# Kernel tuning notes

Measured on AMD Instinct MI355X. Metric: run time of the kernel, lower is better.

Reference implementation:

```python
import jax, jax.numpy as jnp
import numpy as np

NUM_LEVELS = 4
RADIUS = 4


def _avg_pool2(x):
    # x: [N, H, W] -> [N, H//2, W//2], 2x2 mean pool, stride 2 (F.avg_pool2d(corr,2,2))
    N, H, W = x.shape
    return x.reshape(N, H // 2, 2, W // 2, 2).mean(axis=(2, 4))


def _bilinear_sample(img, x, y):
    # img: [N, H, W]; x, y: [N, P] pixel coords.
    # Matches F.grid_sample(..., mode='bilinear', align_corners=True, padding_mode='zeros')
    # after the pixel->normalized->pixel round trip in bilinear_sampler (identity).
    N, H, W = img.shape
    x0 = jnp.floor(x)
    y0 = jnp.floor(y)
    wx = x - x0
    wy = y - y0
    x0i = x0.astype(jnp.int32)
    y0i = y0.astype(jnp.int32)
    flat = img.reshape(N, H * W)

    def gather(yi, xi):
        valid = (xi >= 0) & (xi <= W - 1) & (yi >= 0) & (yi <= H - 1)
        idx = jnp.clip(yi, 0, H - 1) * W + jnp.clip(xi, 0, W - 1)
        v = jnp.take_along_axis(flat, idx, axis=1)
        return jnp.where(valid, v, jnp.zeros((), img.dtype))

    v00 = gather(y0i, x0i)
    v01 = gather(y0i, x0i + 1)
    v10 = gather(y0i + 1, x0i)
    v11 = gather(y0i + 1, x0i + 1)
    return (v00 * (1 - wy) * (1 - wx) + v01 * (1 - wy) * wx
            + v10 * wy * (1 - wx) + v11 * wy * wx)


def _corr_block(fmap1, fmap2, coords):
    B, D, H, W = fmap1.shape
    # all-pairs correlation: [B, H*W, H*W] / sqrt(D)
    f1 = fmap1.reshape(B, D, H * W)
    f2 = fmap2.reshape(B, D, H * W)
    corr = jnp.einsum('bdn,bdm->bnm', f1, f2) / jnp.sqrt(jnp.asarray(D, fmap1.dtype))
    corr = corr.reshape(B * H * W, H, W)
    pyramid = [corr]
    for _ in range(NUM_LEVELS - 1):
        corr = _avg_pool2(corr)
        pyramid.append(corr)

    # coords: [B, 2, H, W] (x, y) -> [B*H*W, 2]
    c = coords.transpose(0, 2, 3, 1).reshape(B * H * W, 2)
    r = RADIUS
    d = jnp.linspace(-r, r, 2 * r + 1)
    dyg, dxg = jnp.meshgrid(d, d, indexing='ij')
    # faithful to torch: delta = stack(meshgrid(dy, dx), -1); channel 0 added to x, 1 to y
    delta = jnp.stack([dyg, dxg], axis=-1).reshape(-1, 2)  # [81, 2]

    outs = []
    for i, lvl in enumerate(pyramid):
        cl = c[:, None, :] / (2.0 ** i) + delta[None, :, :]  # [N, 81, 2]
        s = _bilinear_sample(lvl, cl[..., 0], cl[..., 1])    # [N, 81]
        outs.append(s.reshape(B, H, W, (2 * r + 1) ** 2))
    out = jnp.concatenate(outs, axis=-1)                     # [B, H, W, 4*81]
    return out.transpose(0, 3, 1, 2).astype(jnp.float32)


def setup_inputs() -> dict:
    key = jax.random.key(0)
    k1, k2, k3 = jax.random.split(key, 3)
    B, D, H, W = 2, 256, 80, 80
    fmap1 = jax.random.normal(k1, (B, D, H, W), dtype=jnp.float32)
    fmap2 = jax.random.normal(k2, (B, D, H, W), dtype=jnp.float32)
    # pixel coords in [0, W-1] x [0, H-1] (channel 0 = x, channel 1 = y)
    u = jax.random.uniform(k3, (B, 2, H, W), dtype=jnp.float32)
    scale = jnp.asarray([W - 1, H - 1], jnp.float32).reshape(1, 2, 1, 1)
    coords = u * scale
    return {"fmap1": fmap1, "fmap2": fmap2, "coords": coords}


def reference(fmap1, fmap2, coords):
    return _corr_block(fmap1, fmap2, coords)
```

## Files before the change

kernel.cpp:

```cpp
#include <hip/hip_runtime.h>


typedef _Float16 h2 __attribute__((ext_vector_type(2)));
typedef _Float16 half8 __attribute__((ext_vector_type(8)));
typedef float f32x4 __attribute__((ext_vector_type(4)));

#define HWDIM 80
#define DCH 256
#define NPIX 12800
#define NBUCKET 800
#define CHP 352

__global__ __launch_bounds__(256) void zero_k(float4* __restrict__ dst) {
    int i = blockIdx.x * 256 + threadIdx.x;
    dst[i] = make_float4(0.f, 0.f, 0.f, 0.f);
}

__global__ __launch_bounds__(256) void transpose_all(const float* __restrict__ f1,
                                                     const float* __restrict__ f2,
                                                     _Float16* __restrict__ f1h,
                                                     _Float16* __restrict__ f2p0) {
    __shared__ float tile[256][33];
    int bid = blockIdx.x;
    bool isf1 = bid < 400;
    int lb = isf1 ? bid : bid - 400;
    const float* src = isf1 ? f1 : f2;
    int b = lb / 200;
    int s0 = (lb % 200) * 32;
    int t = threadIdx.x;
    const float* sb = src + (size_t)b * DCH * (HWDIM * HWDIM);
#pragma unroll 4
    for (int k = 0; k < 32; ++k) {
        int j = t + 256 * k;
        int c = j >> 5, s = j & 31;
        tile[c][s] = sb[(size_t)c * (HWDIM * HWDIM) + s0 + s];
    }
    __syncthreads();
    int p = t & 127;
    int srow = t >> 7;
    if (isf1) {
        _Float16* db = f1h + ((size_t)b * 6400 + s0) * DCH;
#pragma unroll 4
        for (int k = 0; k < 16; ++k) {
            int s = 2 * k + srow;
            h2 v;
            v[0] = (_Float16)tile[2 * p][s];
            v[1] = (_Float16)tile[2 * p + 1][s];
            *(h2*)(db + (size_t)s * DCH + 2 * p) = v;
        }
    } else {
#pragma unroll 4
        for (int k = 0; k < 16; ++k) {
            int s = 2 * k + srow;
            int spatial = s0 + s;
            int yy = spatial / 80;
            int xx = spatial - yy * 80;
            h2 v;
            v[0] = (_Float16)tile[2 * p][s];
            v[1] = (_Float16)tile[2 * p + 1][s];
            size_t off = (size_t)b * 2073600 + (size_t)(p >> 4) * 259200
                       + ((size_t)(yy + 5) * 90 + (xx + 5)) * 32 + ((2 * p) & 31);
            *(h2*)(f2p0 + off) = v;
        }
    }
}

__global__ __launch_bounds__(256) void pools(const _Float16* __restrict__ l0,
                                             _Float16* __restrict__ l1,
                                             _Float16* __restrict__ l2,
                                             _Float16* __restrict__ l3) {
    int i = blockIdx.x * 256 + threadIdx.x;
    if (i < 409600) {
        int c2 = i & 15;
        int r = i >> 4;
        int x = r % 40; r /= 40;
        int y = r % 40; r /= 40;
        int pl = r & 7;
        int b = r >> 3;
        const h2* s = (const h2*)l0 + (size_t)b * 1036800 + (size_t)pl * 129600
                    + ((size_t)(2 * y + 5) * 90 + (2 * x + 5)) * 16 + c2;
        h2 v00 = s[0], v01 = s[16], v10 = s[90 * 16], v11 = s[90 * 16 + 16];
        float r0 = ((float)v00[0] + (float)v01[0] + (float)v10[0] + (float)v11[0]) * 0.25f;
        float r1 = ((float)v00[1] + (float)v01[1] + (float)v10[1] + (float)v11[1]) * 0.25f;
        h2 o; o[0] = (_Float16)r0; o[1] = (_Float16)r1;
        *((h2*)l1 + (size_t)b * 320000 + (size_t)pl * 40000
          + ((size_t)(y + 5) * 50 + (x + 5)) * 16 + c2) = o;
    } else if (i < 512000) {
        int j = i - 409600;
        int c2 = j & 15;
        int r = j >> 4;
        int x = r % 20; r /= 20;
        int y = r % 20; r /= 20;
        int pl = r & 7;
        int b = r >> 3;
        const h2* s = (const h2*)l0 + (size_t)b * 1036800 + (size_t)pl * 129600 + c2;
        float r0 = 0.f, r1 = 0.f;
#pragma unroll
        for (int dy = 0; dy < 4; ++dy)
#pragma unroll
            for (int dx = 0; dx < 4; ++dx) {
                h2 v = s[((size_t)(4 * y + dy + 5) * 90 + (4 * x + dx + 5)) * 16];
                r0 += (float)v[0];
                r1 += (float)v[1];
            }
        h2 o; o[0] = (_Float16)(r0 * 0.0625f); o[1] = (_Float16)(r1 * 0.0625f);
        *((h2*)l2 + (size_t)b * 115200 + (size_t)pl * 14400
          + ((size_t)(y + 5) * 30 + (x + 5)) * 16 + c2) = o;
    } else {
        int j = i - 512000;
        int c2 = j & 15;
        int r = j >> 4;
        int x = r % 10; r /= 10;
        int y = r % 10; r /= 10;
        int pl = r & 7;
        int b = r >> 3;
        const h2* s = (const h2*)l0 + (size_t)b * 1036800 + (size_t)pl * 129600 + c2;
        float r0 = 0.f, r1 = 0.f;
#pragma unroll
        for (int dy = 0; dy < 8; ++dy)
#pragma unroll
            for (int dx = 0; dx < 8; ++dx) {
                h2 v = s[((size_t)(8 * y + dy + 5) * 90 + (8 * x + dx + 5)) * 16];
                r0 += (float)v[0];
                r1 += (float)v[1];
            }
        h2 o; o[0] = (_Float16)(r0 * 0.015625f); o[1] = (_Float16)(r1 * 0.015625f);
        *((h2*)l3 + (size_t)b * 51200 + (size_t)pl * 6400
          + ((size_t)(y + 5) * 20 + (x + 5)) * 16 + c2) = o;
    }
}

static __device__ __forceinline__ int bucket_of(const float* coords, int n) {
    int b = n / 6400;
    int r = n - b * 6400;
    float cx = coords[(size_t)b * 12800 + r];
    float cy = coords[(size_t)b * 12800 + 6400 + r];
    int ix = min(max((int)floorf(cx), 0), 79);
    int iy = min(max((int)floorf(cy), 0), 79);
    return b * 400 + (iy >> 2) * 20 + (ix >> 2);
}

__global__ __launch_bounds__(1024) void bucket_k(const float* __restrict__ coords,
                                                 int* __restrict__ sortedIdxP,
                                                 int* __restrict__ rank) {
    __shared__ unsigned int histS[NBUCKET], startS[NBUCKET], curS[NBUCKET];
    __shared__ unsigned int waveSum[16];
    __shared__ unsigned int totalS;
    int t = threadIdx.x;
    if (t < NBUCKET) histS[t] = 0u;
    __syncthreads();
    int bkt[13];
#pragma unroll
    for (int i = 0; i < 13; ++i) {
        int n = i * 1024 + t;
        if (n < NPIX) {
            bkt[i] = bucket_of(coords, n);
            atomicAdd(&histS[bkt[i]], 1u);
        }
    }
    __syncthreads();
    unsigned int v = (t < NBUCKET) ? ((histS[t] + 15u) & ~15u) : 0u;
    unsigned int x = v;
#pragma unroll
    for (int d = 1; d < 64; d <<= 1) {
        unsigned int y = __shfl_up(x, d);
        if ((t & 63) >= d) x += y;
    }
    if ((t & 63) == 63) waveSum[t >> 6] = x;
    __syncthreads();
    if (t < 16) {
        unsigned int w = waveSum[t];
#pragma unroll
        for (int d = 1; d < 16; d <<= 1) {
            unsigned int y = __shfl_up(w, d);
            if (t >= d) w += y;
        }
        waveSum[t] = w;
    }
    __syncthreads();
    unsigned int incl = x + ((t >> 6) ? waveSum[(t >> 6) - 1] : 0u);
    if (t < NBUCKET) {
        unsigned int e = incl - v;
        startS[t] = e;
        curS[t] = e;
        if (t == NBUCKET - 1) totalS = incl;
    }
    __syncthreads();
#pragma unroll
    for (int i = 0; i < 13; ++i) {
        int n = i * 1024 + t;
        if (n < NPIX) {
            unsigned int pos = atomicAdd(&curS[bkt[i]], 1u);
            sortedIdxP[pos] = n;
            rank[n] = (int)pos;
        }
    }
    __syncthreads();
    if (t < NBUCKET) {
        unsigned int h = histS[t];
        if (h) {
            unsigned int pc = (h + 15u) & ~15u;
            unsigned int base = startS[t];
            int dup = sortedIdxP[base];
            for (unsigned int s = h; s < pc; ++s) sortedIdxP[base + s] = dup;
        }
    }
    for (unsigned int s = totalS + t; s < 25600u; s += 1024u) sortedIdxP[s] = -1;
}

template <int L>
static __device__ __forceinline__ void stage_plane(int tid, int wave, int kk,
                                                   const _Float16* __restrict__ f2b,
                                                   char* buf) {
    const int Ww = L == 0 ? 13 : L == 1 ? 11 : 10;
    const int MT = L == 0 ? 169 : L == 1 ? 121 : 100;
    const int MAG = L == 0 ? 161320 : L == 1 ? 190652 : 209716;
    const int Wp = L == 0 ? 90 : L == 1 ? 50 : L == 2 ? 30 : 20;
    const int PSB = 2 * (L == 0 ? 259200 : L == 1 ? 80000 : L == 2 ? 28800 : 12800);
    const int NS = MT * 4;
#pragma unroll
    for (int p = 0; p < (NS + 511) / 512; ++p) {
        int s = p * 512 + tid;
        if (s < NS) {
            int r = s >> 2, c = s & 3;
            int my = (r * MAG) >> 21;
            int mx = r - my * Ww;
            int cc = c ^ (r & 3);
            const char* g = (const char*)f2b + (my * Wp + mx) * 64 + cc * 16 + kk * PSB;
            char* l = buf + (p * 512 + wave * 64) * 16;
            __builtin_amdgcn_global_load_lds(
                (const __attribute__((address_space(1))) void*)g,
                (__attribute__((address_space(3))) void*)l, 16, 0, 0);
        }
    }
}

template <int L>
static __device__ __forceinline__ void run_level(
    int tid, int lane, int wave, int b,
    const _Float16* __restrict__ f2pL,
    const int* X0cS, const int* Y0cS,
    const float (*fxS)[16], const float (*fyS)[16],
    const int (*lxS)[16], const int (*lyS)[16],
    const _Float16* f1S, char (*planeB)[176 * 64], _Float16* G,
    _Float16* __restrict__ sc) {
    const int Ww = L == 0 ? 13 : L == 1 ? 11 : 10;
    const int NT = L == 0 ? 11 : L == 1 ? 8 : 7;
    const int MT = L == 0 ? 169 : L == 1 ? 121 : 100;
    const int Wp = L == 0 ? 90 : L == 1 ? 50 : L == 2 ? 30 : 20;
    const int PB = L == 0 ? 2073600 : L == 1 ? 640000 : L == 2 ? 230400 : 102400;
    const _Float16* f2b = f2pL + (size_t)b * PB
                        + ((size_t)(Y0cS[L] + 5) * Wp + (X0cS[L] + 5)) * 32;
    bool has0 = wave < NT;
    bool has1 = (wave + 8) < NT;
    int ch = lane >> 4;
    int r0 = min(wave * 16 + (lane & 15), MT - 1);
    int r1 = min((wave + 8) * 16 + (lane & 15), MT - 1);
    int la0 = (r0 * 4 + (ch ^ (r0 & 3))) * 16;
    int la1 = (r1 * 4 + (ch ^ (r1 & 3))) * 16;

    f32x4 acc0 = {0.f, 0.f, 0.f, 0.f};
    f32x4 acc1 = {0.f, 0.f, 0.f, 0.f};
    stage_plane<L>(tid, wave, 0, f2b, planeB[0]);
    __syncthreads();
#pragma unroll
    for (int kk = 0; kk < 8; ++kk) {
        if (kk < 7) stage_plane<L>(tid, wave, kk + 1, f2b, planeB[(kk + 1) & 1]);
        half8 bfk = *(const half8*)(f1S + (lane & 15) * 264 + (ch + 4 * kk) * 8);
        const char* pb = planeB[kk & 1];
        if (has0) {
            half8 a0 = *(const half8*)(pb + la0);
            acc0 = __builtin_amdgcn_mfma_f32_16x16x32_f16(a0, bfk, acc0, 0, 0, 0);
        }
        if (has1) {
            half8 a1 = *(const half8*)(pb + la1);
            acc1 = __builtin_amdgcn_mfma_f32_16x16x32_f16(a1, bfk, acc1, 0, 0, 0);
        }
        __syncthreads();
    }
    if (has0) {
        int gr = wave * 16 + ch * 4;
#pragma unroll
        for (int r = 0; r < 4; ++r) G[(gr + r) * 17 + (lane & 15)] = (_Float16)acc0[r];
    }
    if (has1) {
        int gr = (wave + 8) * 16 + ch * 4;
#pragma unroll
        for (int r = 0; r < 4; ++r) G[(gr + r) * 17 + (lane & 15)] = (_Float16)acc1[r];
    }
    __syncthreads();
    for (int idx = tid; idx < 16 * 81; idx += 512) {
        int x = (idx * 12946) >> 20;
        int k = idx - x * 81;
        int a = (k * 57) >> 9;
        int c = k - 9 * a;
        int gx = lxS[L][x] + a, gy = lyS[L][x] + c;
        int m00 = gy * Ww + gx;
        float fx = fxS[L][x], fy = fyS[L][x];
        float t00 = (float)G[m00 * 17 + x];
        float t01 = (float)G[(m00 + 1) * 17 + x];
        float t10 = (float)G[(m00 + Ww) * 17 + x];
        float t11 = (float)G[(m00 + Ww + 1) * 17 + x];
        float v = ((1.f - fy) * ((1.f - fx) * t00 + fx * t01)
                 + fy * ((1.f - fx) * t10 + fx * t11)) * 0.0625f;
        sc[x * CHP + L * 81 + k] = (_Float16)v;
    }
}

__global__ __launch_bounds__(512, 8) void corr_mfma(
    const _Float16* __restrict__ f1h,
    const _Float16* __restrict__ f2p0, const _Float16* __restrict__ f2p1,
    const _Float16* __restrict__ f2p2, const _Float16* __restrict__ f2p3,
    const float* __restrict__ coords, const int* __restrict__ sortedIdxP,
    _Float16* __restrict__ scratch) {
    __shared__ __align__(16) char planeB[2][176 * 64];
    __shared__ _Float16 G[176 * 17];
    __shared__ _Float16 f1S[16 * 264];
    __shared__ float fxS[4][16], fyS[4][16];
    __shared__ int lxS[4][16], lyS[4][16];
    __shared__ int X0cS[4], Y0cS[4], bS;

    int pphys = blockIdx.x;
    int l = (pphys & 7) * 200 + (pphys >> 3);
    int tid = threadIdx.x;
    if (sortedIdxP[l * 16] < 0) return;
    int lane = tid & 63;
    int wave = tid >> 6;

    {
        int px = tid >> 5, q = tid & 31;
        int n = sortedIdxP[l * 16 + px];
        const float4* src = (const float4*)(f1h + (size_t)n * DCH);
        *((float4*)(f1S + px * 264) + q) = src[q];
    }
    if (tid < 64) {
        int px = tid & 15, Lt = tid >> 4;
        int n = sortedIdxP[l * 16 + px];
        int b = n / 6400;
        int r = n - b * 6400;
        float cx = coords[(size_t)b * 12800 + r];
        float cy = coords[(size_t)b * 12800 + 6400 + r];
        float ls = 1.0f / (float)(1 << Lt);
        float cxl = cx * ls, cyl = cy * ls;
        float fxf = floorf(cxl), fyf = floorf(cyl);
        int X0 = (int)fxf - 4, Y0 = (int)fyf - 4;
        int ix = min(max((int)floorf(cx), 0), 79);
        int iy = min(max((int)floorf(cy), 0), 79);
        int X0c = (((ix >> 2) * 4) >> Lt) - 4;
        int Y0c = (((iy >> 2) * 4) >> Lt) - 4;
        lxS[Lt][px] = min(max(X0 - X0c, 0), 3);
        lyS[Lt][px] = min(max(Y0 - Y0c, 0), 3);
        fxS[Lt][px] = cxl - fxf;
        fyS[Lt][px] = cyl - fyf;
        X0cS[Lt] = X0c;
        Y0cS[Lt] = Y0c;
        if (tid == 0) bS = sortedIdxP[l * 16] / 6400;
    }
    __syncthreads();
    int b = bS;
    _Float16* sc = scratch + (size_t)l * 16 * CHP;

    run_level<0>(tid, lane, wave, b, f2p0, X0cS, Y0cS, fxS, fyS, lxS, lyS, f1S, planeB, G, sc);
    run_level<1>(tid, lane, wave, b, f2p1, X0cS, Y0cS, fxS, fyS, lxS, lyS, f1S, planeB, G, sc);
    run_level<2>(tid, lane, wave, b, f2p2, X0cS, Y0cS, fxS, fyS, lxS, lyS, f1S, planeB, G, sc);
    run_level<3>(tid, lane, wave, b, f2p3, X0cS, Y0cS, fxS, fyS, lxS, lyS, f1S, planeB, G, sc);
}

__global__ __launch_bounds__(256) void unsort_t(const _Float16* __restrict__ scratch,
                                                const int* __restrict__ rank,
                                                float* __restrict__ out) {
    __shared__ _Float16 lds[64][40];
    int blk = blockIdx.x;
    int b = blk / 100;
    int nl0 = (blk % 100) * 64;
    int t = threadIdx.x;
    int p = t >> 2, j = t & 3;
    int n = blk * 64 + p;
    int rk = rank[n];
    const float4* src = (const float4*)(scratch + (size_t)rk * CHP);
    int px = t & 63, iq = t >> 6;

    for (int c = 0; c < 11; ++c) {
        float4 f4 = src[c * 4 + j];
        *(float4*)(&lds[p][j * 8]) = f4;
        __syncthreads();
#pragma unroll
        for (int w = 0; w < 8; ++w) {
            int i = w * 4 + iq;
            int ch = c * 32 + i;
            if (ch < 324)
                out[((size_t)b * 324 + ch) * 6400 + nl0 + px] = (float)lds[px][i];
        }
        __syncthreads();
    }
}

extern "C" void kernel_launch(void* const* d_in, const int* in_sizes, int n_in,
                              void* d_out, int out_size, void* d_ws, size_t ws_size,
                              hipStream_t stream) {
    const float* fmap1 = (const float*)d_in[0];
    const float* fmap2 = (const float*)d_in[1];
    const float* coords = (const float*)d_in[2];
    float* out = (float*)d_out;
    char* ws = (char*)d_ws;

    _Float16* f1h  = (_Float16*)(ws);
    _Float16* f2p0 = (_Float16*)(ws + 6553600);
    _Float16* f2p1 = (_Float16*)(ws + 14848000);
    _Float16* f2p2 = (_Float16*)(ws + 17408000);
    _Float16* f2p3 = (_Float16*)(ws + 18329600);
    int* sortedIdxP = (int*)(ws + 18739200);
    int* rank       = (int*)(ws + 18841600);
    _Float16* scratch = (_Float16*)(ws + 18892800);

    zero_k<<<dim3(2975), dim3(256), 0, stream>>>((float4*)f2p0);

    transpose_all<<<dim3(800), dim3(256), 0, stream>>>(fmap1, fmap2, f1h, f2p0);
    pools<<<dim3(2100), dim3(256), 0, stream>>>(f2p0, f2p1, f2p2, f2p3);
    bucket_k<<<dim3(1), dim3(1024), 0, stream>>>(coords, sortedIdxP, rank);
    corr_mfma<<<dim3(1600), dim3(512), 0, stream>>>(f1h, f2p0, f2p1, f2p2, f2p3,
                                                    coords, sortedIdxP, scratch);
    unsort_t<<<dim3(200), dim3(256), 0, stream>>>(scratch, rank, out);
}
```

Baseline: 90.86 us.

## Enlarge pixel buckets to 8x4 and process 32 pixels per correlation block

Coordinate buckets change from 4x4 to 8x4 pixel cells, padded to multiples of 32. Each corr_mfma block now handles 32 query pixels, issuing two MFMAs per staged fmap2 A-fragment so every staged window plane is reused across twice as many pixels. This cuts the global-to-LDS staging traffic per pixel and halves the grid. In exchange each block needs more LDS and larger windows, occupancy is lower (launch bounds 512,2), and the padding per bucket grows.

```diff
diff --git a/kernel.cpp b/kernel.cpp
--- a/kernel.cpp
+++ b/kernel.cpp
@@ -8,7 +8,7 @@
 #define HWDIM 80
 #define DCH 256
 #define NPIX 12800
-#define NBUCKET 800
+#define NBUCKET 400
 #define CHP 352
 
 __global__ __launch_bounds__(256) void zero_k(float4* __restrict__ dst) {
@@ -137,7 +137,7 @@
     float cy = coords[(size_t)b * 12800 + 6400 + r];
     int ix = min(max((int)floorf(cx), 0), 79);
     int iy = min(max((int)floorf(cy), 0), 79);
-    return b * 400 + (iy >> 2) * 20 + (ix >> 2);
+    return b * 200 + (iy >> 3) * 20 + (ix >> 2);
 }
 
 __global__ __launch_bounds__(1024) void bucket_k(const float* __restrict__ coords,
@@ -159,7 +159,7 @@
         }
     }
     __syncthreads();
-    unsigned int v = (t < NBUCKET) ? ((histS[t] + 15u) & ~15u) : 0u;
+    unsigned int v = (t < NBUCKET) ? ((histS[t] + 31u) & ~31u) : 0u;
     unsigned int x = v;
 #pragma unroll
     for (int d = 1; d < 64; d <<= 1) {
@@ -199,7 +199,7 @@
     if (t < NBUCKET) {
         unsigned int h = histS[t];
         if (h) {
-            unsigned int pc = (h + 15u) & ~15u;
+            unsigned int pc = (h + 31u) & ~31u;
             unsigned int base = startS[t];
             int dup = sortedIdxP[base];
             for (unsigned int s = h; s < pc; ++s) sortedIdxP[base + s] = dup;
@@ -213,7 +213,7 @@
                                                    const _Float16* __restrict__ f2b,
                                                    char* buf) {
     const int Ww = L == 0 ? 13 : L == 1 ? 11 : 10;
-    const int MT = L == 0 ? 169 : L == 1 ? 121 : 100;
+    const int MT = L == 0 ? 221 : L == 1 ? 143 : L == 2 ? 110 : 100;
     const int MAG = L == 0 ? 161320 : L == 1 ? 190652 : 209716;
     const int Wp = L == 0 ? 90 : L == 1 ? 50 : L == 2 ? 30 : 20;
     const int PSB = 2 * (L == 0 ? 259200 : L == 1 ? 80000 : L == 2 ? 28800 : 12800);
@@ -240,13 +240,13 @@
     int tid, int lane, int wave, int b,
     const _Float16* __restrict__ f2pL,
     const int* X0cS, const int* Y0cS,
-    const float (*fxS)[16], const float (*fyS)[16],
-    const int (*lxS)[16], const int (*lyS)[16],
-    const _Float16* f1S, char (*planeB)[176 * 64], _Float16* G,
+    const float (*fxS)[32], const float (*fyS)[32],
+    const int (*lxS)[32], const int (*lyS)[32],
+    const _Float16* f1S, char (*planeB)[221 * 64], _Float16* G,
     _Float16* __restrict__ sc) {
     const int Ww = L == 0 ? 13 : L == 1 ? 11 : 10;
-    const int NT = L == 0 ? 11 : L == 1 ? 8 : 7;
-    const int MT = L == 0 ? 169 : L == 1 ? 121 : 100;
+    const int MT = L == 0 ? 221 : L == 1 ? 143 : L == 2 ? 110 : 100;
+    const int NT = (MT + 15) / 16;
     const int Wp = L == 0 ? 90 : L == 1 ? 50 : L == 2 ? 30 : 20;
     const int PB = L == 0 ? 2073600 : L == 1 ? 640000 : L == 2 ? 230400 : 102400;
     const _Float16* f2b = f2pL + (size_t)b * PB
@@ -259,37 +259,48 @@
     int la0 = (r0 * 4 + (ch ^ (r0 & 3))) * 16;
     int la1 = (r1 * 4 + (ch ^ (r1 & 3))) * 16;
 
-    f32x4 acc0 = {0.f, 0.f, 0.f, 0.f};
-    f32x4 acc1 = {0.f, 0.f, 0.f, 0.f};
+    f32x4 acc00 = {0.f, 0.f, 0.f, 0.f};
+    f32x4 acc01 = {0.f, 0.f, 0.f, 0.f};
+    f32x4 acc10 = {0.f, 0.f, 0.f, 0.f};
+    f32x4 acc11 = {0.f, 0.f, 0.f, 0.f};
     stage_plane<L>(tid, wave, 0, f2b, planeB[0]);
     __syncthreads();
 #pragma unroll
     for (int kk = 0; kk < 8; ++kk) {
         if (kk < 7) stage_plane<L>(tid, wave, kk + 1, f2b, planeB[(kk + 1) & 1]);
-        half8 bfk = *(const half8*)(f1S + (lane & 15) * 264 + (ch + 4 * kk) * 8);
+        half8 bf0 = *(const half8*)(f1S + (lane & 15) * 264 + (ch + 4 * kk) * 8);
+        half8 bf1 = *(const half8*)(f1S + (16 + (lane & 15)) * 264 + (ch + 4 * kk) * 8);
         const char* pb = planeB[kk & 1];
         if (has0) {
             half8 a0 = *(const half8*)(pb + la0);
-            acc0 = __builtin_amdgcn_mfma_f32_16x16x32_f16(a0, bfk, acc0, 0, 0, 0);
+            acc00 = __builtin_amdgcn_mfma_f32_16x16x32_f16(a0, bf0, acc00, 0, 0, 0);
+            acc01 = __builtin_amdgcn_mfma_f32_16x16x32_f16(a0, bf1, acc01, 0, 0, 0);
         }
         if (has1) {
             half8 a1 = *(const half8*)(pb + la1);
-            acc1 = __builtin_amdgcn_mfma_f32_16x16x32_f16(a1, bfk, acc1, 0, 0, 0);
+            acc10 = __builtin_amdgcn_mfma_f32_16x16x32_f16(a1, bf0, acc10, 0, 0, 0);
+            acc11 = __builtin_amdgcn_mfma_f32_16x16x32_f16(a1, bf1, acc11, 0, 0, 0);
         }
         __syncthreads();
     }
     if (has0) {
         int gr = wave * 16 + ch * 4;
 #pragma unroll
-        for (int r = 0; r < 4; ++r) G[(gr + r) * 17 + (lane & 15)] = (_Float16)acc0[r];
+        for (int r = 0; r < 4; ++r) {
+            G[(gr + r) * 33 + (lane & 15)] = (_Float16)acc00[r];
+            G[(gr + r) * 33 + 16 + (lane & 15)] = (_Float16)acc01[r];
+        }
     }
     if (has1) {
         int gr = (wave + 8) * 16 + ch * 4;
 #pragma unroll
-        for (int r = 0; r < 4; ++r) G[(gr + r) * 17 + (lane & 15)] = (_Float16)acc1[r];
-    }
-    __syncthreads();
-    for (int idx = tid; idx < 16 * 81; idx += 512) {
+        for (int r = 0; r < 4; ++r) {
+            G[(gr + r) * 33 + (lane & 15)] = (_Float16)acc10[r];
+            G[(gr + r) * 33 + 16 + (lane & 15)] = (_Float16)acc11[r];
+        }
+    }
+    __syncthreads();
+    for (int idx = tid; idx < 32 * 81; idx += 512) {
         int x = (idx * 12946) >> 20;
         int k = idx - x * 81;
         int a = (k * 57) >> 9;
@@ -297,45 +308,48 @@
         int gx = lxS[L][x] + a, gy = lyS[L][x] + c;
         int m00 = gy * Ww + gx;
         float fx = fxS[L][x], fy = fyS[L][x];
-        float t00 = (float)G[m00 * 17 + x];
-        float t01 = (float)G[(m00 + 1) * 17 + x];
-        float t10 = (float)G[(m00 + Ww) * 17 + x];
-        float t11 = (float)G[(m00 + Ww + 1) * 17 + x];
+        float t00 = (float)G[m00 * 33 + x];
+        float t01 = (float)G[(m00 + 1) * 33 + x];
+        float t10 = (float)G[(m00 + Ww) * 33 + x];
+        float t11 = (float)G[(m00 + Ww + 1) * 33 + x];
         float v = ((1.f - fy) * ((1.f - fx) * t00 + fx * t01)
                  + fy * ((1.f - fx) * t10 + fx * t11)) * 0.0625f;
         sc[x * CHP + L * 81 + k] = (_Float16)v;
     }
-}
-
-__global__ __launch_bounds__(512, 8) void corr_mfma(
+    __syncthreads();
+}
+
+__global__ __launch_bounds__(512, 2) void corr_mfma(
     const _Float16* __restrict__ f1h,
     const _Float16* __restrict__ f2p0, const _Float16* __restrict__ f2p1,
     const _Float16* __restrict__ f2p2, const _Float16* __restrict__ f2p3,
     const float* __restrict__ coords, const int* __restrict__ sortedIdxP,
     _Float16* __restrict__ scratch) {
-    __shared__ __align__(16) char planeB[2][176 * 64];
-    __shared__ _Float16 G[176 * 17];
-    __shared__ _Float16 f1S[16 * 264];
-    __shared__ float fxS[4][16], fyS[4][16];
-    __shared__ int lxS[4][16], lyS[4][16];
+    __shared__ __align__(16) char planeB[2][221 * 64];
+    __shared__ _Float16 G[224 * 33];
+    __shared__ _Float16 f1S[32 * 264];
+    __shared__ float fxS[4][32], fyS[4][32];
+    __shared__ int lxS[4][32], lyS[4][32];
     __shared__ int X0cS[4], Y0cS[4], bS;
 
     int pphys = blockIdx.x;
-    int l = (pphys & 7) * 200 + (pphys >> 3);
+    int l = (pphys & 7) * 100 + (pphys >> 3);
     int tid = threadIdx.x;
-    if (sortedIdxP[l * 16] < 0) return;
+    if (sortedIdxP[l * 32] < 0) return;
     int lane = tid & 63;
     int wave = tid >> 6;
 
-    {
-        int px = tid >> 5, q = tid & 31;
-        int n = sortedIdxP[l * 16 + px];
+#pragma unroll
+    for (int uu = 0; uu < 2; ++uu) {
+        int u = tid + uu * 512;
+        int px = u >> 5, q = u & 31;
+        int n = sortedIdxP[l * 32 + px];
         const float4* src = (const float4*)(f1h + (size_t)n * DCH);
         *((float4*)(f1S + px * 264) + q) = src[q];
     }
-    if (tid < 64) {
-        int px = tid & 15, Lt = tid >> 4;
-        int n = sortedIdxP[l * 16 + px];
+    if (tid < 128) {
+        int px = tid & 31, Lt = tid >> 5;
+        int n = sortedIdxP[l * 32 + px];
         int b = n / 6400;
         int r = n - b * 6400;
         float cx = coords[(size_t)b * 12800 + r];
@@ -347,18 +361,19 @@
         int ix = min(max((int)floorf(cx), 0), 79);
         int iy = min(max((int)floorf(cy), 0), 79);
         int X0c = (((ix >> 2) * 4) >> Lt) - 4;
-        int Y0c = (((iy >> 2) * 4) >> Lt) - 4;
+        int Y0c = (((iy >> 3) * 8) >> Lt) - 4;
+        int lyMax = Lt == 0 ? 7 : Lt == 1 ? 3 : Lt == 2 ? 1 : 0;
         lxS[Lt][px] = min(max(X0 - X0c, 0), 3);
-        lyS[Lt][px] = min(max(Y0 - Y0c, 0), 3);
+        lyS[Lt][px] = min(max(Y0 - Y0c, 0), lyMax);
         fxS[Lt][px] = cxl - fxf;
         fyS[Lt][px] = cyl - fyf;
         X0cS[Lt] = X0c;
         Y0cS[Lt] = Y0c;
-        if (tid == 0) bS = sortedIdxP[l * 16] / 6400;
+        if (tid == 0) bS = sortedIdxP[l * 32] / 6400;
     }
     __syncthreads();
     int b = bS;
-    _Float16* sc = scratch + (size_t)l * 16 * CHP;
+    _Float16* sc = scratch + (size_t)l * 32 * CHP;
 
     run_level<0>(tid, lane, wave, b, f2p0, X0cS, Y0cS, fxS, fyS, lxS, lyS, f1S, planeB, G, sc);
     run_level<1>(tid, lane, wave, b, f2p1, X0cS, Y0cS, fxS, fyS, lxS, lyS, f1S, planeB, G, sc);
@@ -418,7 +433,7 @@
     transpose_all<<<dim3(800), dim3(256), 0, stream>>>(fmap1, fmap2, f1h, f2p0);
     pools<<<dim3(2100), dim3(256), 0, stream>>>(f2p0, f2p1, f2p2, f2p3);
     bucket_k<<<dim3(1), dim3(1024), 0, stream>>>(coords, sortedIdxP, rank);
-    corr_mfma<<<dim3(1600), dim3(512), 0, stream>>>(f1h, f2p0, f2p1, f2p2, f2p3,
-                                                    coords, sortedIdxP, scratch);
+    corr_mfma<<<dim3(800), dim3(512), 0, stream>>>(f1h, f2p0, f2p1, f2p2, f2p3,
+                                                   coords, sortedIdxP, scratch);
     unsort_t<<<dim3(200), dim3(256), 0, stream>>>(scratch, rank, out);
 }
```

New measurement: 95.29 us. 1.05x slower.

## Replace block-wide double-buffered staging with per-wave private LDS staging

Applied to the files above, without the earlier changes.

Each wave now loads its own 16-row tile of f2 for all 8 K-slices into a private LDS buffer with global_load_lds, waits on vmcnt, then runs its 8 MFMAs. This removes the per-K-slice block-wide __syncthreads and the shared double buffer. The f1 B-operand fragments are loaded into registers once and reused across all four levels. Launch bounds drop to 2 blocks per CU and LDS use grows to 64KB per block, which lowers occupancy. Each wave also serialises its load and compute, so latency is no longer overlapped within a wave.

```diff
diff --git a/kernel.cpp b/kernel.cpp
--- a/kernel.cpp
+++ b/kernel.cpp
@@ -209,84 +209,49 @@
 }
 
 template <int L>
-static __device__ __forceinline__ void stage_plane(int tid, int wave, int kk,
-                                                   const _Float16* __restrict__ f2b,
-                                                   char* buf) {
-    const int Ww = L == 0 ? 13 : L == 1 ? 11 : 10;
-    const int MT = L == 0 ? 169 : L == 1 ? 121 : 100;
-    const int MAG = L == 0 ? 161320 : L == 1 ? 190652 : 209716;
-    const int Wp = L == 0 ? 90 : L == 1 ? 50 : L == 2 ? 30 : 20;
-    const int PSB = 2 * (L == 0 ? 259200 : L == 1 ? 80000 : L == 2 ? 28800 : 12800);
-    const int NS = MT * 4;
-#pragma unroll
-    for (int p = 0; p < (NS + 511) / 512; ++p) {
-        int s = p * 512 + tid;
-        if (s < NS) {
-            int r = s >> 2, c = s & 3;
-            int my = (r * MAG) >> 21;
-            int mx = r - my * Ww;
-            int cc = c ^ (r & 3);
-            const char* g = (const char*)f2b + (my * Wp + mx) * 64 + cc * 16 + kk * PSB;
-            char* l = buf + (p * 512 + wave * 64) * 16;
-            __builtin_amdgcn_global_load_lds(
-                (const __attribute__((address_space(1))) void*)g,
-                (__attribute__((address_space(3))) void*)l, 16, 0, 0);
-        }
-    }
-}
-
-template <int L>
 static __device__ __forceinline__ void run_level(
     int tid, int lane, int wave, int b,
     const _Float16* __restrict__ f2pL,
     const int* X0cS, const int* Y0cS,
     const float (*fxS)[16], const float (*fyS)[16],
     const int (*lxS)[16], const int (*lyS)[16],
-    const _Float16* f1S, char (*planeB)[176 * 64], _Float16* G,
+    const half8* bf, char* wbuf, _Float16* G,
     _Float16* __restrict__ sc) {
     const int Ww = L == 0 ? 13 : L == 1 ? 11 : 10;
     const int NT = L == 0 ? 11 : L == 1 ? 8 : 7;
     const int MT = L == 0 ? 169 : L == 1 ? 121 : 100;
+    const int MAG = L == 0 ? 161320 : L == 1 ? 190652 : 209716;
     const int Wp = L == 0 ? 90 : L == 1 ? 50 : L == 2 ? 30 : 20;
+    const int PSB = 2 * (L == 0 ? 259200 : L == 1 ? 80000 : L == 2 ? 28800 : 12800);
     const int PB = L == 0 ? 2073600 : L == 1 ? 640000 : L == 2 ? 230400 : 102400;
     const _Float16* f2b = f2pL + (size_t)b * PB
                         + ((size_t)(Y0cS[L] + 5) * Wp + (X0cS[L] + 5)) * 32;
-    bool has0 = wave < NT;
-    bool has1 = (wave + 8) < NT;
+    int rr = lane & 15;
     int ch = lane >> 4;
-    int r0 = min(wave * 16 + (lane & 15), MT - 1);
-    int r1 = min((wave + 8) * 16 + (lane & 15), MT - 1);
-    int la0 = (r0 * 4 + (ch ^ (r0 & 3))) * 16;
-    int la1 = (r1 * 4 + (ch ^ (r1 & 3))) * 16;
-
-    f32x4 acc0 = {0.f, 0.f, 0.f, 0.f};
-    f32x4 acc1 = {0.f, 0.f, 0.f, 0.f};
-    stage_plane<L>(tid, wave, 0, f2b, planeB[0]);
-    __syncthreads();
-#pragma unroll
-    for (int kk = 0; kk < 8; ++kk) {
-        if (kk < 7) stage_plane<L>(tid, wave, kk + 1, f2b, planeB[(kk + 1) & 1]);
-        half8 bfk = *(const half8*)(f1S + (lane & 15) * 264 + (ch + 4 * kk) * 8);
-        const char* pb = planeB[kk & 1];
-        if (has0) {
-            half8 a0 = *(const half8*)(pb + la0);
-            acc0 = __builtin_amdgcn_mfma_f32_16x16x32_f16(a0, bfk, acc0, 0, 0, 0);
-        }
-        if (has1) {
-            half8 a1 = *(const half8*)(pb + la1);
-            acc1 = __builtin_amdgcn_mfma_f32_16x16x32_f16(a1, bfk, acc1, 0, 0, 0);
-        }
-        __syncthreads();
-    }
-    if (has0) {
-        int gr = wave * 16 + ch * 4;
-#pragma unroll
-        for (int r = 0; r < 4; ++r) G[(gr + r) * 17 + (lane & 15)] = (_Float16)acc0[r];
-    }
-    if (has1) {
-        int gr = (wave + 8) * 16 + ch * 4;
-#pragma unroll
-        for (int r = 0; r < 4; ++r) G[(gr + r) * 17 + (lane & 15)] = (_Float16)acc1[r];
+
+    for (int t = wave; t < NT; t += 8) {
+        int r = min(t * 16 + rr, MT - 1);
+        int my = (r * MAG) >> 21;
+        int mx = r - my * Ww;
+        const char* g0 = (const char*)f2b + (my * Wp + mx) * 64 + ch * 16;
+        __builtin_amdgcn_sched_barrier(0);
+#pragma unroll
+        for (int kk = 0; kk < 8; ++kk)
+            __builtin_amdgcn_global_load_lds(
+                (const __attribute__((address_space(1))) void*)(g0 + kk * PSB),
+                (__attribute__((address_space(3))) void*)(wbuf + kk * 1024), 16, 0, 0);
+        asm volatile("s_waitcnt vmcnt(0)" ::: "memory");
+        __builtin_amdgcn_sched_barrier(0);
+        f32x4 acc = {0.f, 0.f, 0.f, 0.f};
+#pragma unroll
+        for (int kk = 0; kk < 8; ++kk) {
+            half8 a = *(const half8*)(wbuf + kk * 1024 + lane * 16);
+            acc = __builtin_amdgcn_mfma_f32_16x16x32_f16(a, bf[kk], acc, 0, 0, 0);
+        }
+        int gr = t * 16 + ch * 4;
+#pragma unroll
+        for (int q = 0; q < 4; ++q)
+            G[(gr + q) * 17 + rr] = (_Float16)acc[q];
     }
     __syncthreads();
     for (int idx = tid; idx < 16 * 81; idx += 512) {
@@ -305,15 +270,16 @@
                  + fy * ((1.f - fx) * t10 + fx * t11)) * 0.0625f;
         sc[x * CHP + L * 81 + k] = (_Float16)v;
     }
-}
-
-__global__ __launch_bounds__(512, 8) void corr_mfma(
+    __syncthreads();
+}
+
+__global__ __launch_bounds__(512, 2) void corr_mfma(
     const _Float16* __restrict__ f1h,
     const _Float16* __restrict__ f2p0, const _Float16* __restrict__ f2p1,
     const _Float16* __restrict__ f2p2, const _Float16* __restrict__ f2p3,
     const float* __restrict__ coords, const int* __restrict__ sortedIdxP,
     _Float16* __restrict__ scratch) {
-    __shared__ __align__(16) char planeB[2][176 * 64];
+    __shared__ __align__(16) char stageB[8][8192];
     __shared__ _Float16 G[176 * 17];
     __shared__ _Float16 f1S[16 * 264];
     __shared__ float fxS[4][16], fyS[4][16];
@@ -359,11 +325,17 @@
     __syncthreads();
     int b = bS;
     _Float16* sc = scratch + (size_t)l * 16 * CHP;
-
-    run_level<0>(tid, lane, wave, b, f2p0, X0cS, Y0cS, fxS, fyS, lxS, lyS, f1S, planeB, G, sc);
-    run_level<1>(tid, lane, wave, b, f2p1, X0cS, Y0cS, fxS, fyS, lxS, lyS, f1S, planeB, G, sc);
-    run_level<2>(tid, lane, wave, b, f2p2, X0cS, Y0cS, fxS, fyS, lxS, lyS, f1S, planeB, G, sc);
-    run_level<3>(tid, lane, wave, b, f2p3, X0cS, Y0cS, fxS, fyS, lxS, lyS, f1S, planeB, G, sc);
+    char* wbuf = stageB[wave];
+
+    half8 bf[8];
+#pragma unroll
+    for (int kk = 0; kk < 8; ++kk)
+        bf[kk] = *(const half8*)(f1S + (lane & 15) * 264 + ((lane >> 4) + 4 * kk) * 8);
+
+    run_level<0>(tid, lane, wave, b, f2p0, X0cS, Y0cS, fxS, fyS, lxS, lyS, bf, wbuf, G, sc);
+    run_level<1>(tid, lane, wave, b, f2p1, X0cS, Y0cS, fxS, fyS, lxS, lyS, bf, wbuf, G, sc);
+    run_level<2>(tid, lane, wave, b, f2p2, X0cS, Y0cS, fxS, fyS, lxS, lyS, bf, wbuf, G, sc);
+    run_level<3>(tid, lane, wave, b, f2p3, X0cS, Y0cS, fxS, fyS, lxS, lyS, bf, wbuf, G, sc);
 }
 
 __global__ __launch_bounds__(256) void unsort_t(const _Float16* __restrict__ scratch,
```

Result: slower. 94.89 us (+4.4%).
